# Kernel tuning notes

Measured on AMD Instinct MI355X. Metric: run time of the kernel, lower is better.

Reference implementation:

```python
import jax, jax.numpy as jnp
import numpy as np

B, S, D, H = 2, 2048, 1024, 16
DH = D // H

def setup_inputs() -> dict:
    key = jax.random.key(0)
    k1, k2, k3, k4 = jax.random.split(key, 4)
    x = jax.random.normal(k1, (B, S, D), dtype=jnp.float32)
    # flax Dense kernels: [in_features, out_features]
    w_qkv = jax.random.normal(k2, (D, 3 * D), dtype=jnp.float32) / np.sqrt(D)
    w_out = jax.random.normal(k3, (D, D), dtype=jnp.float32) / np.sqrt(D)
    b_out = jax.random.normal(k4, (D,), dtype=jnp.float32) * 0.01
    return {"x": x, "w_qkv": w_qkv, "w_out": w_out, "b_out": b_out}

def reference(x, w_qkv, w_out, b_out):
    b, s, d = x.shape
    h, dh = H, d // H
    qkv = jnp.einsum('bsd,de->bse', x, w_qkv)           # [B,S,3D]
    qkv = qkv.reshape(b, s, 3, h, dh)
    qkv = jnp.transpose(qkv, (2, 0, 3, 1, 4))            # [3,B,H,S,DH]
    q, k, v = qkv[0], qkv[1], qkv[2]
    attn = jnp.einsum('bhqd,bhkd->bhqk', q, k) / jnp.sqrt(jnp.float32(dh))
    attn = jax.nn.softmax(attn, axis=-1)                 # [B,H,S,S]
    y = jnp.einsum('bhqk,bhkd->bhqd', attn, v)           # [B,H,S,DH]
    y = jnp.transpose(y, (0, 2, 1, 3)).reshape(b, s, d)  # [B,S,D]
    return jnp.einsum('bsd,de->bse', y, w_out) + b_out
```

## Files before the change

kernel.cpp:

```cpp
#include <hip/hip_runtime.h>
#include <stdint.h>

typedef __bf16 bf16_t;
typedef __bf16 bf16x8 __attribute__((ext_vector_type(8)));
typedef float f32x4 __attribute__((ext_vector_type(4)));
typedef float f32x16 __attribute__((ext_vector_type(16)));
typedef unsigned short u16;
typedef unsigned short u16x8 __attribute__((ext_vector_type(8)));
typedef unsigned int u32;
typedef unsigned int u32x4 __attribute__((ext_vector_type(4)));

#define DEVI __device__ __forceinline__


DEVI u16 bits(float f) { bf16_t h = (bf16_t)f; return __builtin_bit_cast(u16, h); }

DEVI void gld16(const void* g, void* l) {
  __builtin_amdgcn_global_load_lds(
      (const __attribute__((address_space(1))) unsigned int*)g,
      (__attribute__((address_space(3))) unsigned int*)l, 16, 0, 0);
}

DEVI bf16x8 ldsr(const u16* s, int row, int cg) {
  const int byte = row * 128 + ((cg ^ (row & 7)) << 4);
  return *(const bf16x8*)((const char*)s + byte);
}

DEVI bf16x8 ldsrV(const u16* s, int row, int cg) {
  const int byte = row * 256 + ((cg ^ (row & 15)) << 4);
  return *(const bf16x8*)((const char*)s + byte);
}

DEVI float exp2v(float x) { return __builtin_amdgcn_exp2f(x); }

DEVI u32 cvtpk(float lo, float hi) {
  u32 r;
  asm("v_cvt_pk_bf16_f32 %0, %1, %2" : "=v"(r) : "v"(lo), "v"(hi));
  return r;
}

#define MFMA16(a, b, c) __builtin_amdgcn_mfma_f32_16x16x32_bf16(a, b, c, 0, 0, 0)
#define MFMA32(a, b, c) __builtin_amdgcn_mfma_f32_32x32x16_bf16(a, b, c, 0, 0, 0)

#define MKFRAG(dst, S, B)                                              \
  {                                                                    \
    u32 a_ = cvtpk(S[(B) + 0], S[(B) + 1]);                            \
    u32 b_ = cvtpk(S[(B) + 4], S[(B) + 5]);                            \
    u32 c_ = cvtpk(S[(B) + 2], S[(B) + 3]);                            \
    u32 d_ = cvtpk(S[(B) + 6], S[(B) + 7]);                            \
    asm("v_permlane32_swap_b32 %0, %1" : "+v"(a_), "+v"(b_));          \
    asm("v_permlane32_swap_b32 %0, %1" : "+v"(c_), "+v"(d_));          \
    u32x4 u_ = {a_, c_, b_, d_};                                       \
    dst = __builtin_bit_cast(bf16x8, u_);                              \
  }

__global__ void __launch_bounds__(256) cvt8(const float* __restrict__ in,
                                            u16* __restrict__ out, int n8) {
  const int i = blockIdx.x * 256 + threadIdx.x;
  if (i >= n8) return;
  const f32x4* p = (const f32x4*)in;
  const f32x4 a = p[2 * i], b = p[2 * i + 1];
  u16x8 o;
#pragma unroll
  for (int j = 0; j < 4; ++j) { o[j] = bits(a[j]); o[4 + j] = bits(b[j]); }
  *(u16x8*)(out + (size_t)i * 8) = o;
}

__global__ void __launch_bounds__(256) tconv(const float* __restrict__ in,
                                             u16* __restrict__ out, int K, int N) {
  __shared__ float T[64][65];
  const int k0 = blockIdx.x * 64, n0 = blockIdx.y * 64;
  const int tid = threadIdx.x;
#pragma unroll
  for (int i = 0; i < 4; ++i) {
    const int c = i * 256 + tid;
    const int row = c >> 4, c4 = c & 15;
    const f32x4 v = *(const f32x4*)(in + (size_t)(k0 + row) * N + n0 + c4 * 4);
#pragma unroll
    for (int j = 0; j < 4; ++j) T[row][c4 * 4 + j] = v[j];
  }
  __syncthreads();
#pragma unroll
  for (int i = 0; i < 2; ++i) {
    const int c = i * 256 + tid;
    const int nrow = c >> 3, k8 = c & 7;
    u16x8 o;
#pragma unroll
    for (int j = 0; j < 8; ++j) o[j] = bits(T[k8 * 8 + j][nrow]);
    *(u16x8*)(out + (size_t)(n0 + nrow) * K + k0 + k8 * 8) = o;
  }
}

__global__ void __launch_bounds__(256) vtrans(const u16* __restrict__ Vrm,
                                              u16* __restrict__ Vt) {
  __shared__ u16 T[64][72];
  const int s0 = blockIdx.x * 64;
  const int bh = blockIdx.y;
  const int tid = threadIdx.x;
#pragma unroll
  for (int i = 0; i < 2; ++i) {
    const int c = i * 256 + tid, srow = c >> 3, c8 = c & 7;
    const u16x8 v = *(const u16x8*)(Vrm + ((size_t)bh * 2048 + s0 + srow) * 64 + c8 * 8);
#pragma unroll
    for (int j = 0; j < 8; ++j) T[srow][c8 * 8 + j] = v[j];
  }
  __syncthreads();
#pragma unroll
  for (int i = 0; i < 2; ++i) {
    const int c = i * 256 + tid, dr = c >> 3, s8 = c & 7;
    u16x8 o;
#pragma unroll
    for (int j = 0; j < 8; ++j) o[j] = T[s8 * 8 + j][dr];
    *(u16x8*)(Vt + ((size_t)bh * 64 + dr) * 2048 + s0 + s8 * 8) = o;
  }
}

template <int BN>
DEVI void gemm_core(const u16* __restrict__ A, const u16* __restrict__ Bt,
                    u16* As, u16* Bs, int m0, int n0, int Kdim,
                    f32x4 (&acc)[4][BN / 32]) {
  const int NF = BN / 32;
  const int tid = threadIdx.x;
  const int l = tid & 63, w = tid >> 6;
  const int lr = l & 15, lh = l >> 4;
  const int wr = w >> 1, wc = w & 1;
  for (int kt = 0; kt < Kdim; kt += 64) {
#pragma unroll
    for (int i = 0; i < 4; ++i) {
      const int cb = i * 256 + w * 64;
      const int c = cb + l;
      const int row = c >> 3;
      const int col = ((c & 7) ^ (row & 7)) << 3;
      gld16(A + (size_t)(m0 + row) * Kdim + kt + col, As + (size_t)cb * 8);
    }
#pragma unroll
    for (int i = 0; i < BN / 32; ++i) {
      const int cb = i * 256 + w * 64;
      const int c = cb + l;
      const int row = c >> 3;
      const int col = ((c & 7) ^ (row & 7)) << 3;
      gld16(Bt + (size_t)(n0 + row) * Kdim + kt + col, Bs + (size_t)cb * 8);
    }
    __syncthreads();
#pragma unroll
    for (int kk = 0; kk < 2; ++kk) {
      bf16x8 af[4], bfr[NF];
#pragma unroll
      for (int m = 0; m < 4; ++m) af[m] = ldsr(As, wr * 64 + m * 16 + lr, kk * 4 + lh);
#pragma unroll
      for (int n = 0; n < NF; ++n)
        bfr[n] = ldsr(Bs, wc * (BN / 2) + n * 16 + lr, kk * 4 + lh);
#pragma unroll
      for (int m = 0; m < 4; ++m)
#pragma unroll
        for (int n = 0; n < NF; ++n)
          acc[m][n] = MFMA16(af[m], bfr[n], acc[m][n]);
    }
    __syncthreads();
  }
}


DEVI void stage_half(const u16* __restrict__ G, int row0, int kt, u16* dst) {
  const int tid = threadIdx.x;
  const int l = tid & 63, wv = tid >> 6;
  const u16* gp = G + (size_t)row0 * 1024 + kt;
#pragma unroll
  for (int i = 0; i < 2; ++i) {
    const int cb = i * 512 + wv * 64;
    const int c = cb + l;
    const int rih = c >> 3;
    const int col = ((c & 7) ^ (rih & 7)) << 3;
    gld16(gp + (size_t)rih * 1024 + col, dst + cb * 8);
  }
}

template <bool SA1, bool SB2, int VM>
DEVI void qkv_tile(const u16* __restrict__ A, const u16* __restrict__ Bt,
                   int m0, int n0, int ktA1, int ktB2,
                   u16* Ac, u16* Bc, u16* An, f32x4 (&acc)[8][4]) {
  const int tid = threadIdx.x;
  const int l = tid & 63, wv = tid >> 6;
  const int lr = l & 15, lh = l >> 4;
  const int wr = wv >> 2, wc = wv & 3;
  const int ab = wr * 128, bb = wc * 64;
  bf16x8 a0[8], a1[8], b0[4], b1[4];
#pragma unroll
  for (int m = 0; m < 4; ++m)
#pragma unroll
    for (int kk = 0; kk < 2; ++kk)
      a0[m * 2 + kk] = ldsr(Ac, ab + m * 16 + lr, kk * 4 + lh);
#pragma unroll
  for (int n = 0; n < 2; ++n)
#pragma unroll
    for (int kk = 0; kk < 2; ++kk)
      b0[n * 2 + kk] = ldsr(Bc, bb + n * 16 + lr, kk * 4 + lh);
  if (SA1) stage_half(A, m0, ktA1, An);
  __builtin_amdgcn_s_barrier();
  asm volatile("s_waitcnt lgkmcnt(0)" ::: "memory");
  __builtin_amdgcn_sched_barrier(0);
  __builtin_amdgcn_s_setprio(1);
#pragma unroll
  for (int m = 0; m < 4; ++m)
#pragma unroll
    for (int n = 0; n < 2; ++n)
#pragma unroll
      for (int kk = 0; kk < 2; ++kk)
        acc[m][n] = MFMA16(a0[m * 2 + kk], b0[n * 2 + kk], acc[m][n]);
  __builtin_amdgcn_s_setprio(0);
  __builtin_amdgcn_s_barrier();
#pragma unroll
  for (int n = 0; n < 2; ++n)
#pragma unroll
    for (int kk = 0; kk < 2; ++kk)
      b1[n * 2 + kk] = ldsr(Bc, bb + 32 + n * 16 + lr, kk * 4 + lh);
  if (SA1) stage_half(A, m0 + 128, ktA1, An + 8192);
  __builtin_amdgcn_s_barrier();
  asm volatile("s_waitcnt lgkmcnt(0)" ::: "memory");
  __builtin_amdgcn_sched_barrier(0);
  __builtin_amdgcn_s_setprio(1);
#pragma unroll
  for (int m = 0; m < 4; ++m)
#pragma unroll
    for (int n = 0; n < 2; ++n)
#pragma unroll
      for (int kk = 0; kk < 2; ++kk)
        acc[m][2 + n] = MFMA16(a0[m * 2 + kk], b1[n * 2 + kk], acc[m][2 + n]);
  __builtin_amdgcn_s_setprio(0);
  __builtin_amdgcn_s_barrier();
#pragma unroll
  for (int m = 0; m < 4; ++m)
#pragma unroll
    for (int kk = 0; kk < 2; ++kk)
      a1[m * 2 + kk] = ldsr(Ac, ab + 64 + m * 16 + lr, kk * 4 + lh);
  if (SB2) stage_half(Bt, n0, ktB2, Bc);
  __builtin_amdgcn_s_barrier();
  asm volatile("s_waitcnt lgkmcnt(0)" ::: "memory");
  __builtin_amdgcn_sched_barrier(0);
  __builtin_amdgcn_s_setprio(1);
#pragma unroll
  for (int m = 0; m < 4; ++m)
#pragma unroll
    for (int n = 0; n < 2; ++n)
#pragma unroll
      for (int kk = 0; kk < 2; ++kk)
        acc[4 + m][n] = MFMA16(a1[m * 2 + kk], b0[n * 2 + kk], acc[4 + m][n]);
  __builtin_amdgcn_s_setprio(0);
  __builtin_amdgcn_s_barrier();
  if (SB2) stage_half(Bt, n0 + 128, ktB2, Bc + 8192);
  __builtin_amdgcn_s_barrier();
  __builtin_amdgcn_s_setprio(1);
#pragma unroll
  for (int m = 0; m < 4; ++m)
#pragma unroll
    for (int n = 0; n < 2; ++n)
#pragma unroll
      for (int kk = 0; kk < 2; ++kk)
        acc[4 + m][2 + n] = MFMA16(a1[m * 2 + kk], b1[n * 2 + kk], acc[4 + m][2 + n]);
  __builtin_amdgcn_s_setprio(0);
  if (VM == 4) asm volatile("s_waitcnt vmcnt(4)" ::: "memory");
  else if (VM == 0) asm volatile("s_waitcnt vmcnt(0)" ::: "memory");
  __builtin_amdgcn_s_barrier();
}

__global__ void __launch_bounds__(512, 2) gemm_qkv_k(const u16* __restrict__ A,
                                                     const u16* __restrict__ Bt,
                                                     u16* __restrict__ Qb,
                                                     u16* __restrict__ Kb,
                                                     u16* __restrict__ Vb) {
  __shared__ u16 LA[2][16384], LB[2][16384];
  const int bid = blockIdx.x;
  const int g = bid & 7, w24 = bid >> 3;
  const int mt = (g >> 1) * 4 + (w24 & 3);
  const int nt = (g & 1) * 6 + (w24 >> 2);
  const int m0 = mt * 256, n0 = nt * 256;

  stage_half(A, m0, 0, LA[0]);
  stage_half(A, m0 + 128, 0, LA[0] + 8192);
  stage_half(Bt, n0, 0, LB[0]);
  stage_half(Bt, n0 + 128, 0, LB[0] + 8192);
  stage_half(Bt, n0, 64, LB[1]);
  stage_half(Bt, n0 + 128, 64, LB[1] + 8192);
  asm volatile("s_waitcnt vmcnt(4)" ::: "memory");
  __builtin_amdgcn_s_barrier();

  f32x4 acc[8][4] = {};
  u16 *Ac = LA[0], *Bc = LB[0], *An = LA[1], *Bn = LB[1];
#pragma unroll 1
  for (int t = 0; t < 14; ++t) {
    qkv_tile<true, true, 4>(A, Bt, m0, n0, (t + 1) * 64, (t + 2) * 64, Ac, Bc, An, acc);
    u16* tp = Ac; Ac = An; An = tp;
    tp = Bc; Bc = Bn; Bn = tp;
  }
  qkv_tile<true, false, 0>(A, Bt, m0, n0, 15 * 64, 0, Ac, Bc, An, acc);
  { u16* tp = Ac; Ac = An; An = tp; tp = Bc; Bc = Bn; Bn = tp; }
  qkv_tile<false, false, -1>(A, Bt, m0, n0, 0, 0, Ac, Bc, An, acc);

  const int tid = threadIdx.x;
  const int l = tid & 63, wv = tid >> 6;
  const int lr = l & 15, lh = l >> 4;
  const int wr = wv >> 2, wc = wv & 3;
#pragma unroll
  for (int n = 0; n < 4; ++n) {
    const int ng = n0 + wc * 64 + n * 16 + lr;
    const int sel = ng >> 10, h = (ng >> 6) & 15, dh = ng & 63;
    u16* dst = sel == 0 ? Qb : (sel == 1 ? Kb : Vb);
    const float qs = (sel == 0) ? 0.125f * 1.44269504f : 1.0f;
#pragma unroll
    for (int m = 0; m < 8; ++m) {
#pragma unroll
      for (int r = 0; r < 4; ++r) {
        const int mg = m0 + wr * 128 + m * 16 + lh * 4 + r;
        const int b = mg >> 11, s = mg & 2047;
        dst[((size_t)(b * 16 + h) * 2048 + s) * 64 + dh] = bits(acc[m][n][r] * qs);
      }
    }
  }
}

__global__ void __launch_bounds__(256) gemm_out_k(const u16* __restrict__ A,
                                                  const u16* __restrict__ Bt,
                                                  const float* __restrict__ bias,
                                                  float* __restrict__ out) {
  __shared__ u16 As[128 * 64], Bs[64 * 64];
  const int m0 = blockIdx.y * 128, n0 = blockIdx.x * 64;
  f32x4 acc[4][2] = {};
  gemm_core<64>(A, Bt, As, Bs, m0, n0, 1024, acc);
  const int tid = threadIdx.x;
  const int l = tid & 63, w = tid >> 6;
  const int lr = l & 15, lh = l >> 4;
  const int wr = w >> 1, wc = w & 1;
#pragma unroll
  for (int n = 0; n < 2; ++n) {
    const int ng = n0 + wc * 32 + n * 16 + lr;
    const float bv = bias[ng];
#pragma unroll
    for (int m = 0; m < 4; ++m) {
#pragma unroll
      for (int r = 0; r < 4; ++r) {
        const int mg = m0 + wr * 64 + m * 16 + lh * 4 + r;
        out[(size_t)mg * 1024 + ng] = acc[m][n][r] + bv;
      }
    }
  }
}

__global__ void __launch_bounds__(512, 4) attn_k(const u16* __restrict__ Qb,
                                                 const u16* __restrict__ Kb,
                                                 const u16* __restrict__ Vt,
                                                 u16* __restrict__ Yb) {
  __shared__ char smem[65536];
  u16* const KsA = (u16*)smem;
  u16* const KsB = (u16*)(smem + 16384);
  u16* const VsA = (u16*)(smem + 32768);
  u16* const VsB = (u16*)(smem + 49152);

  const int tid = threadIdx.x;
  const int l = tid & 63, w = tid >> 6;
  const int lq = l & 31, hi = l >> 5;
  const int qw = w & 3;
  const int khalf = w >> 2;
  const int i0 = blockIdx.x;
  const int bid = (i0 & 7) * 64 + (i0 >> 3);
  const int bh = bid >> 4, qt = bid & 15;

  const u16* Qp = Qb + ((size_t)bh * 2048 + qt * 128 + qw * 32 + lq) * 64;
  bf16x8 qf0 = *(const bf16x8*)(Qp + hi * 8);
  bf16x8 qf1 = *(const bf16x8*)(Qp + 16 + hi * 8);
  bf16x8 qf2 = *(const bf16x8*)(Qp + 32 + hi * 8);
  bf16x8 qf3 = *(const bf16x8*)(Qp + 48 + hi * 8);

  const u16* Kbase = Kb + (size_t)bh * 2048 * 64;
  const u16* Vbase = Vt + (size_t)bh * 64 * 2048;

  bf16x8 ones;
#pragma unroll
  for (int j = 0; j < 8; ++j) ones[j] = (bf16_t)1.0f;

  f32x16 acc0 = {}, acc1 = {};
  f32x16 accs = {};

#define STAGE(Ksb, Vsb, kv0)                                               \
  {                                                                        \
    _Pragma("unroll") for (int ii = 0; ii < 2; ++ii) {                     \
      const int cb = ii * 512 + w * 64;                                    \
      const int c = cb + l;                                                \
      const int krow = c >> 3;                                             \
      const int kcol = ((c & 7) ^ (krow & 7)) << 3;                        \
      gld16(Kbase + (size_t)((kv0) + krow) * 64 + kcol, (Ksb) + cb * 8);   \
      const int vrow = c >> 4;                                             \
      const int vcol = ((c & 15) ^ (vrow & 15)) << 3;                      \
      gld16(Vbase + (size_t)vrow * 2048 + (kv0) + vcol, (Vsb) + cb * 8);   \
    }                                                                      \
  }

  STAGE(KsA, VsA, 0);
  __syncthreads();
  int cur = 0;

  for (int t = 0; t < 16; ++t) {
    u16* const Ksn = cur ? KsA : KsB;
    u16* const Vsn = cur ? VsA : VsB;
    if (t + 1 < 16) STAGE(Ksn, Vsn, (t + 1) * 128);
    const u16* Ksc = cur ? KsB : KsA;
    const u16* Vsc = cur ? VsB : VsA;

    f32x16 s0 = {}, s1 = {};
    __builtin_amdgcn_s_setprio(1);
#pragma unroll
    for (int ks = 0; ks < 4; ++ks) {
      const bf16x8 qk = ks == 0 ? qf0 : (ks == 1 ? qf1 : (ks == 2 ? qf2 : qf3));
      s0 = MFMA32(ldsr(Ksc, khalf * 64 + lq, ks * 2 + hi), qk, s0);
      s1 = MFMA32(ldsr(Ksc, khalf * 64 + 32 + lq, ks * 2 + hi), qk, s1);
    }
    __builtin_amdgcn_s_setprio(0);

#pragma unroll
    for (int i = 0; i < 16; ++i) { s0[i] = exp2v(s0[i]); s1[i] = exp2v(s1[i]); }

    bf16x8 pa0, pa1, pa2, pa3;
    MKFRAG(pa0, s0, 0);
    MKFRAG(pa1, s0, 8);
    MKFRAG(pa2, s1, 0);
    MKFRAG(pa3, s1, 8);
    __builtin_amdgcn_s_setprio(1);
    accs = MFMA32(pa0, ones, accs);
    acc0 = MFMA32(pa0, ldsrV(Vsc, lq, khalf * 8 + hi), acc0);
    acc1 = MFMA32(pa0, ldsrV(Vsc, 32 + lq, khalf * 8 + hi), acc1);
    accs = MFMA32(pa1, ones, accs);
    acc0 = MFMA32(pa1, ldsrV(Vsc, lq, khalf * 8 + 2 + hi), acc0);
    acc1 = MFMA32(pa1, ldsrV(Vsc, 32 + lq, khalf * 8 + 2 + hi), acc1);
    accs = MFMA32(pa2, ones, accs);
    acc0 = MFMA32(pa2, ldsrV(Vsc, lq, khalf * 8 + 4 + hi), acc0);
    acc1 = MFMA32(pa2, ldsrV(Vsc, 32 + lq, khalf * 8 + 4 + hi), acc1);
    accs = MFMA32(pa3, ones, accs);
    acc0 = MFMA32(pa3, ldsrV(Vsc, lq, khalf * 8 + 6 + hi), acc0);
    acc1 = MFMA32(pa3, ldsrV(Vsc, 32 + lq, khalf * 8 + 6 + hi), acc1);
    __builtin_amdgcn_s_setprio(0);

    __syncthreads();
    cur ^= 1;
  }
#undef STAGE

  float* const F = (float*)smem;
  float* const Fp = F + (size_t)(tid & 255) * 49;
  if (khalf) {
#pragma unroll
    for (int r = 0; r < 16; ++r) {
      Fp[r] = acc0[r];
      Fp[16 + r] = acc1[r];
      Fp[32 + r] = accs[r];
    }
  }
  __syncthreads();
  if (khalf) return;
#pragma unroll
  for (int r = 0; r < 16; ++r) {
    acc0[r] += Fp[r];
    acc1[r] += Fp[16 + r];
    accs[r] += Fp[32 + r];
  }

  const int b = bh >> 4, h = bh & 15;
#pragma unroll
  for (int r = 0; r < 16; ++r) {
    const float sd = 1.0f / accs[r];
    const int row = (r & 3) + 8 * (r >> 2) + 4 * hi;
    const int sq = qt * 128 + qw * 32 + row;
    u16* yp = Yb + ((size_t)b * 2048 + sq) * 1024 + h * 64;
    yp[lq] = bits(acc0[r] * sd);
    yp[32 + lq] = bits(acc1[r] * sd);
  }
}

extern "C" void kernel_launch(void* const* d_in, const int* in_sizes, int n_in,
                              void* d_out, int out_size, void* d_ws, size_t ws_size,
                              hipStream_t stream) {
  (void)in_sizes; (void)n_in; (void)out_size; (void)ws_size;
  const float* x     = (const float*)d_in[0];
  const float* w_qkv = (const float*)d_in[1];
  const float* w_out = (const float*)d_in[2];
  const float* b_out = (const float*)d_in[3];
  float* out = (float*)d_out;

  char* ws = (char*)d_ws;
  u16* xb    = (u16*)(ws);
  u16* wqkvT = (u16*)(ws + 8388608);
  u16* woutT = (u16*)(ws + 14680064);
  u16* Qb    = (u16*)(ws + 16777216);
  u16* Kb    = (u16*)(ws + 25165824);
  u16* Vrm   = (u16*)(ws + 33554432);
  u16* Vt    = (u16*)(ws + 41943040);
  u16* Yb    = xb;

  cvt8<<<2048, 256, 0, stream>>>(x, xb, 4194304 / 8);
  tconv<<<dim3(16, 48), 256, 0, stream>>>(w_qkv, wqkvT, 1024, 3072);
  tconv<<<dim3(16, 16), 256, 0, stream>>>(w_out, woutT, 1024, 1024);
  gemm_qkv_k<<<192, 512, 0, stream>>>(xb, wqkvT, Qb, Kb, Vrm);
  vtrans<<<dim3(32, 32), 256, 0, stream>>>(Vrm, Vt);
  attn_k<<<512, 512, 0, stream>>>(Qb, Kb, Vt, Yb);
  gemm_out_k<<<dim3(16, 32), 256, 0, stream>>>(Yb, woutT, b_out, out);
}
```

Baseline: 112.7 us.

## Software-pipeline attention loop, deferring second-half PV MFMAs into the next iteration

Restructures the flash-attention inner loop so the PV MFMAs for the second half of each key tile run at the start of the next iteration, before the barrier and the next prefetch. Exp2 calls are interleaved between QK and PV MFMAs so transcendental work overlaps matrix instructions. The end-of-iteration __syncthreads is replaced by an explicit vmcnt wait plus s_barrier placed after the deferred MFMAs, and the loop is kept rolled. This lengthens buffer lifetimes (the previous V buffer must stay valid until the barrier) and adds register pressure from the carried fragments.

Result: no change. 111.7 us (-0.8%).

```diff
diff --git a/kernel.cpp b/kernel.cpp
--- a/kernel.cpp
+++ b/kernel.cpp
@@ -395,53 +395,81 @@
   }
 
   STAGE(KsA, VsA, 0);
-  __syncthreads();
+  asm volatile("s_waitcnt vmcnt(0)" ::: "memory");
+  __builtin_amdgcn_s_barrier();
+
+  bf16x8 pc0 = ones, pc1 = ones;
   int cur = 0;
-
+#pragma unroll 1
   for (int t = 0; t < 16; ++t) {
-    u16* const Ksn = cur ? KsA : KsB;
-    u16* const Vsn = cur ? VsA : VsB;
-    if (t + 1 < 16) STAGE(Ksn, Vsn, (t + 1) * 128);
     const u16* Ksc = cur ? KsB : KsA;
     const u16* Vsc = cur ? VsB : VsA;
+    const u16* Vsp = cur ? VsA : VsB;
+
+    if (t > 0) {
+      __builtin_amdgcn_s_setprio(1);
+      accs = MFMA32(pc0, ones, accs);
+      acc0 = MFMA32(pc0, ldsrV(Vsp, lq, khalf * 8 + 4 + hi), acc0);
+      acc1 = MFMA32(pc0, ldsrV(Vsp, 32 + lq, khalf * 8 + 4 + hi), acc1);
+      accs = MFMA32(pc1, ones, accs);
+      acc0 = MFMA32(pc1, ldsrV(Vsp, lq, khalf * 8 + 6 + hi), acc0);
+      acc1 = MFMA32(pc1, ldsrV(Vsp, 32 + lq, khalf * 8 + 6 + hi), acc1);
+      __builtin_amdgcn_s_setprio(0);
+      asm volatile("s_waitcnt vmcnt(0)" ::: "memory");
+      __builtin_amdgcn_s_barrier();
+    }
+    if (t + 1 < 16) STAGE((cur ? KsA : KsB), (cur ? VsA : VsB), (t + 1) * 128);
 
     f32x16 s0 = {}, s1 = {};
     __builtin_amdgcn_s_setprio(1);
-#pragma unroll
-    for (int ks = 0; ks < 4; ++ks) {
-      const bf16x8 qk = ks == 0 ? qf0 : (ks == 1 ? qf1 : (ks == 2 ? qf2 : qf3));
-      s0 = MFMA32(ldsr(Ksc, khalf * 64 + lq, ks * 2 + hi), qk, s0);
-      s1 = MFMA32(ldsr(Ksc, khalf * 64 + 32 + lq, ks * 2 + hi), qk, s1);
-    }
+    s0 = MFMA32(ldsr(Ksc, khalf * 64 + lq, hi), qf0, s0);
+    s0 = MFMA32(ldsr(Ksc, khalf * 64 + lq, 2 + hi), qf1, s0);
+    s0 = MFMA32(ldsr(Ksc, khalf * 64 + lq, 4 + hi), qf2, s0);
+    s0 = MFMA32(ldsr(Ksc, khalf * 64 + lq, 6 + hi), qf3, s0);
+    s1 = MFMA32(ldsr(Ksc, khalf * 64 + 32 + lq, hi), qf0, s1);
+    s0[0] = exp2v(s0[0]); s0[1] = exp2v(s0[1]); s0[2] = exp2v(s0[2]); s0[3] = exp2v(s0[3]);
+    s1 = MFMA32(ldsr(Ksc, khalf * 64 + 32 + lq, 2 + hi), qf1, s1);
+    s0[4] = exp2v(s0[4]); s0[5] = exp2v(s0[5]); s0[6] = exp2v(s0[6]); s0[7] = exp2v(s0[7]);
+    s1 = MFMA32(ldsr(Ksc, khalf * 64 + 32 + lq, 4 + hi), qf2, s1);
+    s0[8] = exp2v(s0[8]); s0[9] = exp2v(s0[9]); s0[10] = exp2v(s0[10]); s0[11] = exp2v(s0[11]);
+    s1 = MFMA32(ldsr(Ksc, khalf * 64 + 32 + lq, 6 + hi), qf3, s1);
+    s0[12] = exp2v(s0[12]); s0[13] = exp2v(s0[13]); s0[14] = exp2v(s0[14]); s0[15] = exp2v(s0[15]);
     __builtin_amdgcn_s_setprio(0);
 
-#pragma unroll
-    for (int i = 0; i < 16; ++i) { s0[i] = exp2v(s0[i]); s1[i] = exp2v(s1[i]); }
-
-    bf16x8 pa0, pa1, pa2, pa3;
+    bf16x8 pa0, pa1;
     MKFRAG(pa0, s0, 0);
     MKFRAG(pa1, s0, 8);
-    MKFRAG(pa2, s1, 0);
-    MKFRAG(pa3, s1, 8);
+
     __builtin_amdgcn_s_setprio(1);
     accs = MFMA32(pa0, ones, accs);
+    s1[0] = exp2v(s1[0]); s1[1] = exp2v(s1[1]); s1[2] = exp2v(s1[2]);
     acc0 = MFMA32(pa0, ldsrV(Vsc, lq, khalf * 8 + hi), acc0);
+    s1[3] = exp2v(s1[3]); s1[4] = exp2v(s1[4]); s1[5] = exp2v(s1[5]);
     acc1 = MFMA32(pa0, ldsrV(Vsc, 32 + lq, khalf * 8 + hi), acc1);
+    s1[6] = exp2v(s1[6]); s1[7] = exp2v(s1[7]); s1[8] = exp2v(s1[8]);
     accs = MFMA32(pa1, ones, accs);
+    s1[9] = exp2v(s1[9]); s1[10] = exp2v(s1[10]); s1[11] = exp2v(s1[11]);
     acc0 = MFMA32(pa1, ldsrV(Vsc, lq, khalf * 8 + 2 + hi), acc0);
+    s1[12] = exp2v(s1[12]); s1[13] = exp2v(s1[13]); s1[14] = exp2v(s1[14]);
     acc1 = MFMA32(pa1, ldsrV(Vsc, 32 + lq, khalf * 8 + 2 + hi), acc1);
-    accs = MFMA32(pa2, ones, accs);
-    acc0 = MFMA32(pa2, ldsrV(Vsc, lq, khalf * 8 + 4 + hi), acc0);
-    acc1 = MFMA32(pa2, ldsrV(Vsc, 32 + lq, khalf * 8 + 4 + hi), acc1);
-    accs = MFMA32(pa3, ones, accs);
-    acc0 = MFMA32(pa3, ldsrV(Vsc, lq, khalf * 8 + 6 + hi), acc0);
-    acc1 = MFMA32(pa3, ldsrV(Vsc, 32 + lq, khalf * 8 + 6 + hi), acc1);
+    s1[15] = exp2v(s1[15]);
     __builtin_amdgcn_s_setprio(0);
 
-    __syncthreads();
+    MKFRAG(pc0, s1, 0);
+    MKFRAG(pc1, s1, 8);
     cur ^= 1;
   }
+  {
+    const u16* Vsp = cur ? VsA : VsB;
+    accs = MFMA32(pc0, ones, accs);
+    acc0 = MFMA32(pc0, ldsrV(Vsp, lq, khalf * 8 + 4 + hi), acc0);
+    acc1 = MFMA32(pc0, ldsrV(Vsp, 32 + lq, khalf * 8 + 4 + hi), acc1);
+    accs = MFMA32(pc1, ones, accs);
+    acc0 = MFMA32(pc1, ldsrV(Vsp, lq, khalf * 8 + 6 + hi), acc0);
+    acc1 = MFMA32(pc1, ldsrV(Vsp, 32 + lq, khalf * 8 + 6 + hi), acc1);
+  }
 #undef STAGE
+  __syncthreads();
 
   float* const F = (float*)smem;
   float* const Fp = F + (size_t)(tid & 255) * 49;
```
